# Optimization experiments

Measured on AMD Instinct MI355X. Metric: run time of the kernel, lower is better.

## Reference

```python
import jax, jax.numpy as jnp
import numpy as np

FEATURE = 256
HIDDEN = 256

def setup_inputs() -> dict:
    key = jax.random.key(0)
    k1, k2, k3 = jax.random.split(key, 3)
    x = jax.random.normal(k1, (64, 2048, FEATURE), dtype=jnp.float32)
    # xavier_normal with gain=0.1: std = 0.1 * sqrt(2/(fan_in+fan_out))
    std_x = 0.1 * np.sqrt(2.0 / (FEATURE + 4 * HIDDEN))
    std_h = 0.1 * np.sqrt(2.0 / (HIDDEN + 4 * HIDDEN))
    WeightX = jax.random.normal(k2, (FEATURE, 4 * HIDDEN), dtype=jnp.float32) * std_x
    WeightH = jax.random.normal(k3, (HIDDEN, 4 * HIDDEN), dtype=jnp.float32) * std_h
    BiasX = jnp.zeros((4 * HIDDEN,), dtype=jnp.float32)
    BiasH = jnp.zeros((4 * HIDDEN,), dtype=jnp.float32)
    return {"x": x, "WeightX": WeightX, "WeightH": WeightH, "BiasX": BiasX, "BiasH": BiasH}

def reference(x, WeightX, WeightH, BiasX, BiasH):
    bs, T, _ = x.shape
    H = WeightH.shape[0]
    # precompute input projection for all timesteps: (bs, T, 4H)
    x_proj = jnp.einsum('btf,fg->btg', x, WeightX) + BiasX + BiasH

    def step(carry, xp_t):
        h, c = carry
        gates = xp_t + h @ WeightH  # (bs, 4H)
        i = jax.nn.sigmoid(gates[:, :H])
        f = jax.nn.sigmoid(gates[:, H:2 * H])
        g = jnp.tanh(gates[:, 2 * H:3 * H])
        o = jax.nn.sigmoid(gates[:, 3 * H:])
        c = f * c + i * g
        h = o * jnp.tanh(c)
        return (h, c), h

    h0 = jnp.zeros((bs, H), dtype=x.dtype)
    c0 = jnp.zeros((bs, H), dtype=x.dtype)
    (h_n, _), out_t = jax.lax.scan(step, (h0, c0), jnp.swapaxes(x_proj, 0, 1))
    output = jnp.swapaxes(out_t, 0, 1)  # (bs, T, H)
    return output, h_n
```

## Files before the change

kernel.cpp:

```cpp
#include <hip/hip_runtime.h>
#include <hip/hip_fp16.h>

#define BATCH 64
#define TSEQ  2048
#define FEAT  256
#define HID   256
#define G4    1024

typedef _Float16 half2_t __attribute__((ext_vector_type(2)));

__device__ __forceinline__ float dot2acc_u(unsigned int a, unsigned int b, float acc) {
    half2_t ah = __builtin_bit_cast(half2_t, a);
    half2_t bh = __builtin_bit_cast(half2_t, b);
#if __has_builtin(__builtin_amdgcn_fdot2)
    return __builtin_amdgcn_fdot2(ah, bh, acc, false);
#else
    return acc + (float)ah.x * (float)bh.x + (float)ah.y * (float)bh.y;
#endif
}

__device__ __forceinline__ float sig_f(float x)  { return 1.f / (1.f + __expf(-x)); }
__device__ __forceinline__ float tanh_f(float x) { return 1.f - 2.f / (__expf(2.f * x) + 1.f); }

__device__ __forceinline__ unsigned int pack2(float a, float b) {
    half2_t h = { (_Float16)a, (_Float16)b };
    return __builtin_bit_cast(unsigned int, h);
}

template <int CTRL>
__device__ __forceinline__ float dpp_add(float x) {
    int y = __builtin_amdgcn_update_dpp(0, __builtin_bit_cast(int, x), CTRL, 0xf, 0xf, true);
    return x + __builtin_bit_cast(float, y);
}

__global__ void wt_convert(const float* __restrict__ WH, uint4* __restrict__ WS,
                           uint4* __restrict__ WST) {
    int idx = blockIdx.x * 256 + threadIdx.x;
    int u = idx >> 13;
    int r = idx & 8191;
    int p = r >> 9;
    int tid = r & 511;
    int w = tid >> 6, c = (tid >> 3) & 7, s = tid & 7;
    int j = p * 64 + w * 8 + c;
    int k0 = 32 * s + 8 * u;
    uint4 v;
    v.x = pack2(WH[(k0 + 0) * G4 + j], WH[(k0 + 1) * G4 + j]);
    v.y = pack2(WH[(k0 + 2) * G4 + j], WH[(k0 + 3) * G4 + j]);
    v.z = pack2(WH[(k0 + 4) * G4 + j], WH[(k0 + 5) * G4 + j]);
    v.w = pack2(WH[(k0 + 6) * G4 + j], WH[(k0 + 7) * G4 + j]);
    if (p < 12) {
        WS[u * 8192 + p * 512 + tid] = v;
    } else {
        int q = p - 12;
        WST[(q * 4 + u) * 512 + tid] = v;
    }
}

__global__ __launch_bounds__(256) void xproj_gemm(
    const float* __restrict__ X, const float* __restrict__ WX,
    const float* __restrict__ BX, const float* __restrict__ BH,
    _Float16* __restrict__ XP)
{
    __shared__ float As[64][17];
    __shared__ float Bs[16][68];

    const int tid = threadIdx.x;
    const int tx = tid & 15;
    const int ty = tid >> 4;
    const int rowBase = blockIdx.y * 64;
    const int colBase = blockIdx.x * 64;

    const int ea = tid * 4;
    const int ar = ea >> 4, ac = ea & 15;
    const int br = ea >> 6, bc = ea & 63;

    float acc[4][4] = {};

    for (int kt = 0; kt < FEAT; kt += 16) {
        float4 av = *(const float4*)(X  + (size_t)(rowBase + ar) * FEAT + kt + ac);
        float4 bv = *(const float4*)(WX + (size_t)(kt + br) * G4 + colBase + bc);
        As[ar][ac + 0] = av.x; As[ar][ac + 1] = av.y;
        As[ar][ac + 2] = av.z; As[ar][ac + 3] = av.w;
        *(float4*)&Bs[br][bc] = bv;
        __syncthreads();
        #pragma unroll
        for (int kk = 0; kk < 16; ++kk) {
            float4 b = *(const float4*)&Bs[kk][tx * 4];
            float a0 = As[ty * 4 + 0][kk];
            float a1 = As[ty * 4 + 1][kk];
            float a2 = As[ty * 4 + 2][kk];
            float a3 = As[ty * 4 + 3][kk];
            acc[0][0] = fmaf(a0, b.x, acc[0][0]); acc[0][1] = fmaf(a0, b.y, acc[0][1]);
            acc[0][2] = fmaf(a0, b.z, acc[0][2]); acc[0][3] = fmaf(a0, b.w, acc[0][3]);
            acc[1][0] = fmaf(a1, b.x, acc[1][0]); acc[1][1] = fmaf(a1, b.y, acc[1][1]);
            acc[1][2] = fmaf(a1, b.z, acc[1][2]); acc[1][3] = fmaf(a1, b.w, acc[1][3]);
            acc[2][0] = fmaf(a2, b.x, acc[2][0]); acc[2][1] = fmaf(a2, b.y, acc[2][1]);
            acc[2][2] = fmaf(a2, b.z, acc[2][2]); acc[2][3] = fmaf(a2, b.w, acc[2][3]);
            acc[3][0] = fmaf(a3, b.x, acc[3][0]); acc[3][1] = fmaf(a3, b.y, acc[3][1]);
            acc[3][2] = fmaf(a3, b.z, acc[3][2]); acc[3][3] = fmaf(a3, b.w, acc[3][3]);
        }
        __syncthreads();
    }

    const int n0 = colBase + tx * 4;
    float4 bxv = *(const float4*)(BX + n0);
    float4 bhv = *(const float4*)(BH + n0);
    float bb0 = bxv.x + bhv.x, bb1 = bxv.y + bhv.y;
    float bb2 = bxv.z + bhv.z, bb3 = bxv.w + bhv.w;

    #pragma unroll
    for (int i = 0; i < 4; ++i) {
        int row = rowBase + ty * 4 + i;
        _Float16* p = XP + (size_t)row * G4 + n0;
        half2_t p01 = { (_Float16)(acc[i][0] + bb0), (_Float16)(acc[i][1] + bb1) };
        half2_t p23 = { (_Float16)(acc[i][2] + bb2), (_Float16)(acc[i][3] + bb3) };
        *(half2_t*)(p + 0) = p01;
        *(half2_t*)(p + 2) = p23;
    }
}

#define DO_PASS(P, W0, W1, W2, W3)                                              \
    {                                                                           \
        float a0_ = 0.f, a1_ = 0.f;                                             \
        a0_ = dot2acc_u(hr0.x, (W0).x, a0_); a0_ = dot2acc_u(hr0.y, (W0).y, a0_); \
        a0_ = dot2acc_u(hr0.z, (W0).z, a0_); a0_ = dot2acc_u(hr0.w, (W0).w, a0_); \
        a1_ = dot2acc_u(hr1.x, (W1).x, a1_); a1_ = dot2acc_u(hr1.y, (W1).y, a1_); \
        a1_ = dot2acc_u(hr1.z, (W1).z, a1_); a1_ = dot2acc_u(hr1.w, (W1).w, a1_); \
        a0_ = dot2acc_u(hr2.x, (W2).x, a0_); a0_ = dot2acc_u(hr2.y, (W2).y, a0_); \
        a0_ = dot2acc_u(hr2.z, (W2).z, a0_); a0_ = dot2acc_u(hr2.w, (W2).w, a0_); \
        a1_ = dot2acc_u(hr3.x, (W3).x, a1_); a1_ = dot2acc_u(hr3.y, (W3).y, a1_); \
        a1_ = dot2acc_u(hr3.z, (W3).z, a1_); a1_ = dot2acc_u(hr3.w, (W3).w, a1_); \
        float acc = a0_ + a1_;                                                  \
        acc = dpp_add<0xB1>(acc);                                               \
        acc = dpp_add<0x4E>(acc);                                               \
        acc = dpp_add<0x141>(acc);                                              \
        if (s == 0) g_sh[(P) * 64 + w * 8 + c] = acc;                           \
    }

#define LDS_PASS(PP)                                                            \
    {                                                                           \
        uint4 l0 = LDS_W[((PP) * 4 + 0) * 512 + tid];                           \
        uint4 l1 = LDS_W[((PP) * 4 + 1) * 512 + tid];                           \
        uint4 l2 = LDS_W[((PP) * 4 + 2) * 512 + tid];                           \
        uint4 l3 = LDS_W[((PP) * 4 + 3) * 512 + tid];                           \
        DO_PASS(9 + (PP), l0, l1, l2, l3);                                      \
    }

__global__ __launch_bounds__(512, 2) void lstm_rec(
    const _Float16* __restrict__ XP, const uint4* __restrict__ WS,
    const uint4* __restrict__ WST, float* __restrict__ OUT)
{
    __shared__ uint4 LDS_W[3 * 4 * 512];
    __shared__ float g_sh[G4];
    __shared__ __align__(16) unsigned short hs[4][64];

    const int tid = threadIdx.x;
    const int b = blockIdx.x;
    const int w = tid >> 6;
    const int c = (tid >> 3) & 7;
    const int s = tid & 7;

    uint4 wreg[36];
    #pragma unroll
    for (int p = 0; p < 9; ++p) {
        #pragma unroll
        for (int u = 0; u < 4; ++u)
            wreg[p * 4 + u] = WS[u * 8192 + p * 512 + tid];
    }
    #pragma unroll
    for (int i = 0; i < 36; ++i)
        asm volatile("" : "+v"(wreg[i].x), "+v"(wreg[i].y),
                          "+v"(wreg[i].z), "+v"(wreg[i].w));

    #pragma unroll
    for (int pp = 0; pp < 3; ++pp) {
        #pragma unroll
        for (int u = 0; u < 4; ++u)
            LDS_W[(pp * 4 + u) * 512 + tid] = WS[u * 8192 + (9 + pp) * 512 + tid];
    }

    if (tid < 256) ((unsigned short*)hs)[tid] = 0;
    float cst = 0.f, hlast = 0.f;
    const _Float16* xpb = XP + (size_t)b * TSEQ * G4;
    float* outb = OUT + (size_t)b * TSEQ * HID;

    float xv0 = 0.f, xv1 = 0.f, xv2 = 0.f, xv3 = 0.f;
    if (tid < 256) {
        xv0 = (float)xpb[tid];       xv1 = (float)xpb[tid + 256];
        xv2 = (float)xpb[tid + 512]; xv3 = (float)xpb[tid + 768];
    }
    __syncthreads();

    #pragma unroll 1
    for (int t = 0; t < TSEQ; ++t) {
        uint4 hr0 = ((const uint4*)(&hs[0][0]))[s];
        uint4 hr1 = ((const uint4*)(&hs[1][0]))[s];
        uint4 hr2 = ((const uint4*)(&hs[2][0]))[s];
        uint4 hr3 = ((const uint4*)(&hs[3][0]))[s];

        uintptr_t stb_i = (uintptr_t)WST;
        asm volatile("" : "+s"(stb_i));
        const uint4* stb = (const uint4*)stb_i;

        uint4 pf0 = stb[(0 * 4 + 0) * 512 + tid];
        uint4 pf1 = stb[(0 * 4 + 1) * 512 + tid];
        uint4 pf2 = stb[(0 * 4 + 2) * 512 + tid];
        uint4 pf3 = stb[(0 * 4 + 3) * 512 + tid];

        DO_PASS(0, wreg[0],  wreg[1],  wreg[2],  wreg[3]);
        DO_PASS(1, wreg[4],  wreg[5],  wreg[6],  wreg[7]);
        DO_PASS(2, wreg[8],  wreg[9],  wreg[10], wreg[11]);
        DO_PASS(3, wreg[12], wreg[13], wreg[14], wreg[15]);

        DO_PASS(12, pf0, pf1, pf2, pf3);
        pf0 = stb[(1 * 4 + 0) * 512 + tid];
        pf1 = stb[(1 * 4 + 1) * 512 + tid];
        pf2 = stb[(1 * 4 + 2) * 512 + tid];
        pf3 = stb[(1 * 4 + 3) * 512 + tid];

        DO_PASS(4, wreg[16], wreg[17], wreg[18], wreg[19]);
        DO_PASS(5, wreg[20], wreg[21], wreg[22], wreg[23]);
        DO_PASS(6, wreg[24], wreg[25], wreg[26], wreg[27]);

        DO_PASS(13, pf0, pf1, pf2, pf3);
        pf0 = stb[(2 * 4 + 0) * 512 + tid];
        pf1 = stb[(2 * 4 + 1) * 512 + tid];
        pf2 = stb[(2 * 4 + 2) * 512 + tid];
        pf3 = stb[(2 * 4 + 3) * 512 + tid];

        DO_PASS(7, wreg[28], wreg[29], wreg[30], wreg[31]);
        DO_PASS(8, wreg[32], wreg[33], wreg[34], wreg[35]);
        LDS_PASS(0);

        DO_PASS(14, pf0, pf1, pf2, pf3);
        pf0 = stb[(3 * 4 + 0) * 512 + tid];
        pf1 = stb[(3 * 4 + 1) * 512 + tid];
        pf2 = stb[(3 * 4 + 2) * 512 + tid];
        pf3 = stb[(3 * 4 + 3) * 512 + tid];

        float xn0 = 0.f, xn1 = 0.f, xn2 = 0.f, xn3 = 0.f;
        {
            int tn = (t + 1 < TSEQ) ? (t + 1) : t;
            if (tid < 256) {
                const _Float16* xq = xpb + (size_t)tn * G4;
                xn0 = (float)xq[tid];       xn1 = (float)xq[tid + 256];
                xn2 = (float)xq[tid + 512]; xn3 = (float)xq[tid + 768];
            }
        }

        LDS_PASS(1);
        LDS_PASS(2);
        DO_PASS(15, pf0, pf1, pf2, pf3);

        __syncthreads();

        if (tid < 256) {
            float gi = sig_f(g_sh[tid] + xv0);
            float gf = sig_f(g_sh[tid + 256] + xv1);
            float gg = tanh_f(g_sh[tid + 512] + xv2);
            float go = sig_f(g_sh[tid + 768] + xv3);
            cst = gf * cst + gi * gg;
            float h = go * tanh_f(cst);
            outb[(size_t)t * HID + tid] = h;
            hlast = h;
            hs[(tid >> 3) & 3][(tid >> 5) * 8 + (tid & 7)] =
                __builtin_bit_cast(unsigned short, (_Float16)h);
        }
        xv0 = xn0; xv1 = xn1; xv2 = xn2; xv3 = xn3;
        __syncthreads();
    }

    if (tid < 256)
        OUT[(size_t)BATCH * TSEQ * HID + (size_t)b * HID + tid] = hlast;
}

extern "C" void kernel_launch(void* const* d_in, const int* in_sizes, int n_in,
                              void* d_out, int out_size, void* d_ws, size_t ws_size,
                              hipStream_t stream) {
    const float* x  = (const float*)d_in[0];
    const float* wx = (const float*)d_in[1];
    const float* wh = (const float*)d_in[2];
    const float* bx = (const float*)d_in[3];
    const float* bh = (const float*)d_in[4];
    float* out = (float*)d_out;

    _Float16* xp = (_Float16*)d_ws;
    uint4* ws = (uint4*)((char*)d_ws + (size_t)BATCH * TSEQ * G4 * sizeof(_Float16));
    uint4* wst = ws + 32768;

    hipLaunchKernelGGL(wt_convert, dim3(128), dim3(256), 0, stream, wh, ws, wst);
    hipLaunchKernelGGL(xproj_gemm, dim3(G4 / 64, (BATCH * TSEQ) / 64), dim3(256), 0, stream,
                       x, wx, bx, bh, xp);
    hipLaunchKernelGGL(lstm_rec, dim3(BATCH), dim3(512), 0, stream, xp, ws, wst, out);
}
```

Baseline: 6.410 ms.

## Keep recurrent weights in AGPRs and enlarge LDS-resident weight share

```diff
diff --git a/kernel.cpp b/kernel.cpp
--- a/kernel.cpp
+++ b/kernel.cpp
@@ -33,8 +33,7 @@
     return x + __builtin_bit_cast(float, y);
 }
 
-__global__ void wt_convert(const float* __restrict__ WH, uint4* __restrict__ WS,
-                           uint4* __restrict__ WST) {
+__global__ void wt_convert(const float* __restrict__ WH, uint4* __restrict__ WS) {
     int idx = blockIdx.x * 256 + threadIdx.x;
     int u = idx >> 13;
     int r = idx & 8191;
@@ -48,12 +47,7 @@
     v.y = pack2(WH[(k0 + 2) * G4 + j], WH[(k0 + 3) * G4 + j]);
     v.z = pack2(WH[(k0 + 4) * G4 + j], WH[(k0 + 5) * G4 + j]);
     v.w = pack2(WH[(k0 + 6) * G4 + j], WH[(k0 + 7) * G4 + j]);
-    if (p < 12) {
-        WS[u * 8192 + p * 512 + tid] = v;
-    } else {
-        int q = p - 12;
-        WST[(q * 4 + u) * 512 + tid] = v;
-    }
+    WS[u * 8192 + p * 512 + tid] = v;
 }
 
 __global__ __launch_bounds__(256) void xproj_gemm(
@@ -137,20 +131,49 @@
         if (s == 0) g_sh[(P) * 64 + w * 8 + c] = acc;                           \
     }
 
+#define AG_RD(d, a_) asm("v_accvgpr_read_b32 %0, %1" : "=v"(d) : "a"(a_), "s"(t))
+
+#define AG_PASS(P)                                                              \
+    {                                                                           \
+        unsigned int t0, t1, t2, t3, t4, t5, t6, t7;                            \
+        float a0_ = 0.f, a1_ = 0.f;                                             \
+        AG_RD(t0, wa[(P)*4 + 0].x); AG_RD(t1, wa[(P)*4 + 0].y);                 \
+        AG_RD(t2, wa[(P)*4 + 0].z); AG_RD(t3, wa[(P)*4 + 0].w);                 \
+        AG_RD(t4, wa[(P)*4 + 1].x); AG_RD(t5, wa[(P)*4 + 1].y);                 \
+        AG_RD(t6, wa[(P)*4 + 1].z); AG_RD(t7, wa[(P)*4 + 1].w);                 \
+        a0_ = dot2acc_u(hr0.x, t0, a0_); a0_ = dot2acc_u(hr0.y, t1, a0_);       \
+        a0_ = dot2acc_u(hr0.z, t2, a0_); a0_ = dot2acc_u(hr0.w, t3, a0_);       \
+        a1_ = dot2acc_u(hr1.x, t4, a1_); a1_ = dot2acc_u(hr1.y, t5, a1_);       \
+        a1_ = dot2acc_u(hr1.z, t6, a1_); a1_ = dot2acc_u(hr1.w, t7, a1_);       \
+        AG_RD(t0, wa[(P)*4 + 2].x); AG_RD(t1, wa[(P)*4 + 2].y);                 \
+        AG_RD(t2, wa[(P)*4 + 2].z); AG_RD(t3, wa[(P)*4 + 2].w);                 \
+        AG_RD(t4, wa[(P)*4 + 3].x); AG_RD(t5, wa[(P)*4 + 3].y);                 \
+        AG_RD(t6, wa[(P)*4 + 3].z); AG_RD(t7, wa[(P)*4 + 3].w);                 \
+        a0_ = dot2acc_u(hr2.x, t0, a0_); a0_ = dot2acc_u(hr2.y, t1, a0_);       \
+        a0_ = dot2acc_u(hr2.z, t2, a0_); a0_ = dot2acc_u(hr2.w, t3, a0_);       \
+        a1_ = dot2acc_u(hr3.x, t4, a1_); a1_ = dot2acc_u(hr3.y, t5, a1_);       \
+        a1_ = dot2acc_u(hr3.z, t6, a1_); a1_ = dot2acc_u(hr3.w, t7, a1_);       \
+        float acc = a0_ + a1_;                                                  \
+        acc = dpp_add<0xB1>(acc);                                               \
+        acc = dpp_add<0x4E>(acc);                                               \
+        acc = dpp_add<0x141>(acc);                                              \
+        if (s == 0) g_sh[(P) * 64 + w * 8 + c] = acc;                           \
+    }
+
 #define LDS_PASS(PP)                                                            \
     {                                                                           \
         uint4 l0 = LDS_W[((PP) * 4 + 0) * 512 + tid];                           \
         uint4 l1 = LDS_W[((PP) * 4 + 1) * 512 + tid];                           \
         uint4 l2 = LDS_W[((PP) * 4 + 2) * 512 + tid];                           \
         uint4 l3 = LDS_W[((PP) * 4 + 3) * 512 + tid];                           \
-        DO_PASS(9 + (PP), l0, l1, l2, l3);                                      \
+        DO_PASS(10 + (PP), l0, l1, l2, l3);                                     \
     }
 
 __global__ __launch_bounds__(512, 2) void lstm_rec(
     const _Float16* __restrict__ XP, const uint4* __restrict__ WS,
-    const uint4* __restrict__ WST, float* __restrict__ OUT)
+    float* __restrict__ OUT)
 {
-    __shared__ uint4 LDS_W[3 * 4 * 512];
+    __shared__ uint4 LDS_W[4 * 4 * 512];
     __shared__ float g_sh[G4];
     __shared__ __align__(16) unsigned short hs[4][64];
 
@@ -160,23 +183,24 @@
     const int c = (tid >> 3) & 7;
     const int s = tid & 7;
 
-    uint4 wreg[36];
+    uint4 wa[40];
     #pragma unroll
-    for (int p = 0; p < 9; ++p) {
+    for (int p = 0; p < 10; ++p) {
+        #pragma unroll
+        for (int u = 0; u < 4; ++u) {
+            uint4 v = WS[u * 8192 + p * 512 + tid];
+            asm("v_accvgpr_write_b32 %0, %1" : "=a"(wa[p * 4 + u].x) : "v"(v.x));
+            asm("v_accvgpr_write_b32 %0, %1" : "=a"(wa[p * 4 + u].y) : "v"(v.y));
+            asm("v_accvgpr_write_b32 %0, %1" : "=a"(wa[p * 4 + u].z) : "v"(v.z));
+            asm("v_accvgpr_write_b32 %0, %1" : "=a"(wa[p * 4 + u].w) : "v"(v.w));
+        }
+    }
+
+    #pragma unroll
+    for (int pp = 0; pp < 4; ++pp) {
         #pragma unroll
         for (int u = 0; u < 4; ++u)
-            wreg[p * 4 + u] = WS[u * 8192 + p * 512 + tid];
-    }
-    #pragma unroll
-    for (int i = 0; i < 36; ++i)
-        asm volatile("" : "+v"(wreg[i].x), "+v"(wreg[i].y),
-                          "+v"(wreg[i].z), "+v"(wreg[i].w));
-
-    #pragma unroll
-    for (int pp = 0; pp < 3; ++pp) {
-        #pragma unroll
-        for (int u = 0; u < 4; ++u)
-            LDS_W[(pp * 4 + u) * 512 + tid] = WS[u * 8192 + (9 + pp) * 512 + tid];
+            LDS_W[(pp * 4 + u) * 512 + tid] = WS[u * 8192 + (10 + pp) * 512 + tid];
     }
 
     if (tid < 256) ((unsigned short*)hs)[tid] = 0;
@@ -198,45 +222,32 @@
         uint4 hr2 = ((const uint4*)(&hs[2][0]))[s];
         uint4 hr3 = ((const uint4*)(&hs[3][0]))[s];
 
-        uintptr_t stb_i = (uintptr_t)WST;
+        uintptr_t stb_i = (uintptr_t)WS;
         asm volatile("" : "+s"(stb_i));
         const uint4* stb = (const uint4*)stb_i;
 
-        uint4 pf0 = stb[(0 * 4 + 0) * 512 + tid];
-        uint4 pf1 = stb[(0 * 4 + 1) * 512 + tid];
-        uint4 pf2 = stb[(0 * 4 + 2) * 512 + tid];
-        uint4 pf3 = stb[(0 * 4 + 3) * 512 + tid];
-
-        DO_PASS(0, wreg[0],  wreg[1],  wreg[2],  wreg[3]);
-        DO_PASS(1, wreg[4],  wreg[5],  wreg[6],  wreg[7]);
-        DO_PASS(2, wreg[8],  wreg[9],  wreg[10], wreg[11]);
-        DO_PASS(3, wreg[12], wreg[13], wreg[14], wreg[15]);
-
-        DO_PASS(12, pf0, pf1, pf2, pf3);
-        pf0 = stb[(1 * 4 + 0) * 512 + tid];
-        pf1 = stb[(1 * 4 + 1) * 512 + tid];
-        pf2 = stb[(1 * 4 + 2) * 512 + tid];
-        pf3 = stb[(1 * 4 + 3) * 512 + tid];
-
-        DO_PASS(4, wreg[16], wreg[17], wreg[18], wreg[19]);
-        DO_PASS(5, wreg[20], wreg[21], wreg[22], wreg[23]);
-        DO_PASS(6, wreg[24], wreg[25], wreg[26], wreg[27]);
-
-        DO_PASS(13, pf0, pf1, pf2, pf3);
-        pf0 = stb[(2 * 4 + 0) * 512 + tid];
-        pf1 = stb[(2 * 4 + 1) * 512 + tid];
-        pf2 = stb[(2 * 4 + 2) * 512 + tid];
-        pf3 = stb[(2 * 4 + 3) * 512 + tid];
-
-        DO_PASS(7, wreg[28], wreg[29], wreg[30], wreg[31]);
-        DO_PASS(8, wreg[32], wreg[33], wreg[34], wreg[35]);
+        uint4 pf0 = stb[0 * 8192 + 14 * 512 + tid];
+        uint4 pf1 = stb[1 * 8192 + 14 * 512 + tid];
+        uint4 pf2 = stb[2 * 8192 + 14 * 512 + tid];
+        uint4 pf3 = stb[3 * 8192 + 14 * 512 + tid];
+
+        AG_PASS(0);
+        AG_PASS(1);
+        AG_PASS(2);
         LDS_PASS(0);
+        AG_PASS(3);
+        AG_PASS(4);
+        AG_PASS(5);
 
         DO_PASS(14, pf0, pf1, pf2, pf3);
-        pf0 = stb[(3 * 4 + 0) * 512 + tid];
-        pf1 = stb[(3 * 4 + 1) * 512 + tid];
-        pf2 = stb[(3 * 4 + 2) * 512 + tid];
-        pf3 = stb[(3 * 4 + 3) * 512 + tid];
+        pf0 = stb[0 * 8192 + 15 * 512 + tid];
+        pf1 = stb[1 * 8192 + 15 * 512 + tid];
+        pf2 = stb[2 * 8192 + 15 * 512 + tid];
+        pf3 = stb[3 * 8192 + 15 * 512 + tid];
+
+        AG_PASS(6);
+        AG_PASS(7);
+        LDS_PASS(1);
 
         float xn0 = 0.f, xn1 = 0.f, xn2 = 0.f, xn3 = 0.f;
         {
@@ -248,8 +259,10 @@
             }
         }
 
-        LDS_PASS(1);
+        AG_PASS(8);
+        AG_PASS(9);
         LDS_PASS(2);
+        LDS_PASS(3);
         DO_PASS(15, pf0, pf1, pf2, pf3);
 
         __syncthreads();
@@ -286,10 +299,9 @@
 
     _Float16* xp = (_Float16*)d_ws;
     uint4* ws = (uint4*)((char*)d_ws + (size_t)BATCH * TSEQ * G4 * sizeof(_Float16));
-    uint4* wst = ws + 32768;
-
-    hipLaunchKernelGGL(wt_convert, dim3(128), dim3(256), 0, stream, wh, ws, wst);
+
+    hipLaunchKernelGGL(wt_convert, dim3(128), dim3(256), 0, stream, wh, ws);
     hipLaunchKernelGGL(xproj_gemm, dim3(G4 / 64, (BATCH * TSEQ) / 64), dim3(256), 0, stream,
                        x, wx, bx, bh, xp);
-    hipLaunchKernelGGL(lstm_rec, dim3(BATCH), dim3(512), 0, stream, xp, ws, wst, out);
-}
+    hipLaunchKernelGGL(lstm_rec, dim3(BATCH), dim3(512), 0, stream, xp, ws, out);
+}
```

After: 6.999 ms. 9.2% more time.
